# Kernel optimization log

Hardware: AMD Instinct MI355X
Metric: run time of the kernel (lower is better)

The kernel has to match this reference:

```python
import jax, jax.numpy as jnp
import numpy as np

HEADS = 8
DIM_HEAD = 64
NB_FEATURES = 256
CHUNK = 128          # chunk size used by performer's causal_linear_attention_noncuda
EPS_KERNEL = 1e-4    # eps in softmax_kernel feature map
EPS_DENOM = 1e-6     # eps added to k_cumsum in the denominator


def softmax_kernel(data, proj, is_query):
    # FAVOR+ positive softmax random features (performer_pytorch.softmax_kernel)
    # data: [B,H,N,D], proj: [M,D]
    d = data.shape[-1]
    normalizer = d ** -0.25
    ratio = proj.shape[0] ** -0.5
    data_dash = jnp.einsum('bhnd,md->bhnm', data * normalizer, proj)
    # ||x||^2 / (2*sqrt(d))
    diag = jnp.sum(data * data, axis=-1, keepdims=True) * 0.5 * (normalizer ** 2)
    if is_query:
        m = jax.lax.stop_gradient(jnp.max(data_dash, axis=-1, keepdims=True))
    else:
        m = jax.lax.stop_gradient(jnp.max(data_dash, axis=(-1, -2), keepdims=True))
    return ratio * (jnp.exp(data_dash - diag - m) + EPS_KERNEL)


def causal_linear_attention(qp, kp, v, chunk=CHUNK):
    # Chunked causal linear attention (O(N) in seq len):
    # out_i = q'_i . S_i / (q'_i . z_i), S_i = sum_{j<=i} k'_j v_j^T, z_i = cumsum k'_j
    B, H, N, M = qp.shape
    E = v.shape[-1]
    C = N // chunk

    def to_chunks(x):
        return x.reshape(B, H, C, chunk, x.shape[-1]).transpose(2, 0, 1, 3, 4)

    qc, kc, vc = to_chunks(qp), to_chunks(kp), to_chunks(v)
    k0 = jnp.zeros((B, H, M), qp.dtype)
    s0 = jnp.zeros((B, H, M, E), qp.dtype)

    def step(carry, inp):
        k_last, s_last = carry
        q, k, vv = inp  # [B,H,c,M], [B,H,c,M], [B,H,c,E]
        k_cum = k_last[:, :, None, :] + jnp.cumsum(k, axis=2)           # [B,H,c,M]
        d_inv = 1.0 / jnp.einsum('bhnm,bhnm->bhn', q, k_cum + EPS_DENOM)
        ctx = jnp.einsum('bhnm,bhne->bhnme', k, vv)                      # [B,H,c,M,E]
        s_cum = s_last[:, :, None] + jnp.cumsum(ctx, axis=2)             # [B,H,c,M,E]
        out = jnp.einsum('bhnme,bhnm,bhn->bhne', s_cum, q, d_inv)        # [B,H,c,E]
        return (k_cum[:, :, -1, :], s_cum[:, :, -1]), out

    _, outs = jax.lax.scan(step, (k0, s0), (qc, kc, vc))  # [C,B,H,c,E]
    return outs.transpose(1, 2, 0, 3, 4).reshape(B, H, N, E)


def setup_inputs() -> dict:
    key = jax.random.key(0)
    k1, k2, k3, k4 = jax.random.split(key, 4)
    B, N, D = 4, 2048, 512
    return {
        'query': jax.random.normal(k1, (B, N, D), jnp.float32),
        'key': jax.random.normal(k2, (B, N, D), jnp.float32),
        'value': jax.random.normal(k3, (B, N, D), jnp.float32),
        'projection': jax.random.normal(k4, (NB_FEATURES, DIM_HEAD), jnp.float32),
    }


def reference(query, key, value, projection):
    B, N, D = query.shape

    def split(x):  # [B,N,D] -> [B,H,N,Dh]
        return x.reshape(B, N, HEADS, DIM_HEAD).transpose(0, 2, 1, 3)

    q, k, v = split(query), split(key), split(value)
    qp = softmax_kernel(q, projection, is_query=True)
    kp = softmax_kernel(k, projection, is_query=False)
    out = causal_linear_attention(qp, kp, v)
    return out.transpose(0, 2, 1, 3).reshape(B, N, D)
```

## Files before the change

kernel.cpp:

```cpp
#include <hip/hip_runtime.h>
#include <math.h>

#define BB 4
#define NN 2048
#define DD 512
#define HH 8
#define DH 64
#define MM 256
#define BH 32
#define CHK 128
#define NCH 16
#define ROWS (BH*NN)

constexpr float NRM   = 0.35355339059327373f;
constexpr float RATIO = 0.0625f;
constexpr float EPSK  = 1e-4f;
constexpr float EPSD  = 1e-6f;

#define OFFB_QP   ((size_t)0)
#define OFFB_SP   ((size_t)33554432)
#define OFFB_KP   (OFFB_SP + (size_t)16777216)
#define OFFB_VT   (OFFB_KP + (size_t)33554432)
#define OFFB_Z    (OFFB_VT + (size_t)8388608)
#define OFFB_KMP  (OFFB_Z  + (size_t)524288)
#define OFFB_KMAX (OFFB_KMP + (size_t)4096)

typedef __attribute__((ext_vector_type(8))) short short8;
typedef __attribute__((ext_vector_type(4))) float f32x4;

__device__ __forceinline__ float b2f(ushort u) {
  union { float f; unsigned int i; } x; x.i = ((unsigned int)u) << 16; return x.f;
}
__device__ __forceinline__ ushort f2b(float f) {
  unsigned int u = __float_as_uint(f);
  unsigned int r = (u + 0x7FFFu + ((u >> 16) & 1u)) >> 16;
  return (ushort)r;
}

#define MFMA(a,b,c) __builtin_amdgcn_mfma_f32_16x16x32_bf16(a, b, c, 0, 0, 0)

template<int MODE>
__global__ __launch_bounds__(256) void featm_kernel(const float* __restrict__ inp,
                                                    const float* __restrict__ proj,
                                                    char* __restrict__ ws) {
  __shared__ __align__(16) char lds[55296];
  __shared__ float diag_s[64];
  __shared__ __align__(16) float wmax[64][4];
  __shared__ float kred[4];

  ushort* xh = (ushort*)lds;
  ushort* xl = xh + 64*72;
  ushort* ps = xl + 64*72;
  ushort* qt = ps;

  const int t  = threadIdx.x;
  const int w  = t >> 6;
  const int l  = t & 63;
  const int lq = l >> 4;
  const int ln = l & 15;

  const int rowbase = blockIdx.x * 64;
  const int bh = rowbase >> 11;
  const int b  = bh >> 3, h = bh & 7;
  const int n0 = rowbase & (NN - 1);

  {
    const int r  = t >> 2;
    const int c0 = (t & 3) * 16;
    const float* src = inp + ((size_t)(b*NN + n0 + r))*DD + h*DH + c0;
    float vv[16];
    #pragma unroll
    for (int j = 0; j < 4; ++j) {
      float4 v = *(const float4*)(src + j*4);
      vv[4*j+0] = v.x*NRM; vv[4*j+1] = v.y*NRM;
      vv[4*j+2] = v.z*NRM; vv[4*j+3] = v.w*NRM;
    }
    float s = 0.f;
    ushort hi[16], lo[16];
    #pragma unroll
    for (int j = 0; j < 16; ++j) {
      s += vv[j]*vv[j];
      hi[j] = f2b(vv[j]);
      lo[j] = f2b(vv[j] - b2f(hi[j]));
    }
    *(short8*)(xh + r*72 + c0)     = *(short8*)&hi[0];
    *(short8*)(xh + r*72 + c0 + 8) = *(short8*)&hi[8];
    *(short8*)(xl + r*72 + c0)     = *(short8*)&lo[0];
    *(short8*)(xl + r*72 + c0 + 8) = *(short8*)&lo[8];
    s += __shfl_xor(s, 1); s += __shfl_xor(s, 2);
    if ((t & 3) == 0) diag_s[r] = 0.5f * s;
  }
  #pragma unroll
  for (int ld = 0; ld < 4; ++ld) {
    int flat = t + 256*ld;
    int r = flat >> 2, c0 = (flat & 3) * 16;
    const float* src = proj + (size_t)r*DH + c0;
    ushort hv[16];
    #pragma unroll
    for (int j = 0; j < 4; ++j) {
      float4 v = *(const float4*)(src + j*4);
      hv[4*j+0] = f2b(v.x); hv[4*j+1] = f2b(v.y);
      hv[4*j+2] = f2b(v.z); hv[4*j+3] = f2b(v.w);
    }
    *(short8*)(ps + r*72 + c0)     = *(short8*)&hv[0];
    *(short8*)(ps + r*72 + c0 + 8) = *(short8*)&hv[8];
  }
  __syncthreads();

  f32x4 acc[4][4];
  #pragma unroll
  for (int mt = 0; mt < 4; ++mt)
    #pragma unroll
    for (int nt = 0; nt < 4; ++nt) acc[mt][nt] = (f32x4){0.f,0.f,0.f,0.f};

  #pragma unroll
  for (int kk = 0; kk < 2; ++kk) {
    short8 ah[4], al[4];
    #pragma unroll
    for (int mt = 0; mt < 4; ++mt) {
      ah[mt] = *(const short8*)(xh + (mt*16 + ln)*72 + kk*32 + lq*8);
      al[mt] = *(const short8*)(xl + (mt*16 + ln)*72 + kk*32 + lq*8);
    }
    #pragma unroll
    for (int nt = 0; nt < 4; ++nt) {
      short8 bf = *(const short8*)(ps + (w*64 + nt*16 + ln)*72 + kk*32 + lq*8);
      #pragma unroll
      for (int mt = 0; mt < 4; ++mt) {
        acc[mt][nt] = MFMA(al[mt], bf, acc[mt][nt]);
        acc[mt][nt] = MFMA(ah[mt], bf, acc[mt][nt]);
      }
    }
  }

  if (MODE == 1) {
    float mx = -1e30f;
    #pragma unroll
    for (int mt = 0; mt < 4; ++mt)
      #pragma unroll
      for (int nt = 0; nt < 4; ++nt)
        #pragma unroll
        for (int reg = 0; reg < 4; ++reg) mx = fmaxf(mx, acc[mt][nt][reg]);
    #pragma unroll
    for (int m = 1; m < 64; m <<= 1) mx = fmaxf(mx, __shfl_xor(mx, m));
    if (l == 0) kred[w] = mx;
    __syncthreads();
    if (t == 0)
      ((float*)(ws + OFFB_KMP))[blockIdx.x] =
        fmaxf(fmaxf(kred[0], kred[1]), fmaxf(kred[2], kred[3]));
    return;
  }

  if (MODE == 0) {
    #pragma unroll
    for (int mt = 0; mt < 4; ++mt)
      #pragma unroll
      for (int reg = 0; reg < 4; ++reg) {
        float m = acc[mt][0][reg];
        #pragma unroll
        for (int nt = 1; nt < 4; ++nt) m = fmaxf(m, acc[mt][nt][reg]);
        m = fmaxf(m, __shfl_xor(m, 1));
        m = fmaxf(m, __shfl_xor(m, 2));
        m = fmaxf(m, __shfl_xor(m, 4));
        m = fmaxf(m, __shfl_xor(m, 8));
        if (ln == 0) wmax[mt*16 + lq*4 + reg][w] = m;
      }
  }
  __syncthreads();

  float km = 0.f;
  if (MODE == 2) km = ((const float*)(ws + OFFB_KMAX))[bh];

  #pragma unroll
  for (int mt = 0; mt < 4; ++mt)
    #pragma unroll
    for (int reg = 0; reg < 4; ++reg) {
      const int row = mt*16 + lq*4 + reg;
      float rm;
      if (MODE == 0) {
        float4 wm4 = *(const float4*)&wmax[row][0];
        rm = fmaxf(fmaxf(wm4.x, wm4.y), fmaxf(wm4.z, wm4.w));
      } else {
        rm = km;
      }
      const float dg = diag_s[row];
      #pragma unroll
      for (int nt = 0; nt < 4; ++nt)
        qt[row*264 + w*64 + nt*16 + ln] =
          f2b(RATIO*(expf(acc[mt][nt][reg] - dg - rm) + EPSK));
    }
  __syncthreads();

  ushort* dstbase = (ushort*)(ws + (MODE == 0 ? OFFB_QP : OFFB_KP)) + (size_t)rowbase*MM;
  #pragma unroll
  for (int ld = 0; ld < 8; ++ld) {
    int flat = t + 256*ld;
    int row = flat >> 5, g = flat & 31;
    *(short8*)(dstbase + (size_t)row*MM + g*8) = *(const short8*)(qt + row*264 + g*8);
  }
}

__global__ void kmax_kernel(char* __restrict__ ws) {
  const int t = threadIdx.x;
  if (t < BH) {
    const float* kmp = (const float*)(ws + OFFB_KMP);
    float m = -1e30f;
    for (int i = 0; i < 32; ++i) m = fmaxf(m, kmp[t*32 + i]);
    ((float*)(ws + OFFB_KMAX))[t] = m;
  }
}

__global__ __launch_bounds__(256) void vt_kernel(const float* __restrict__ value,
                                                 char* __restrict__ ws) {
  __shared__ __align__(16) float vsh[128][68];
  const int t = threadIdx.x;
  const int bh = blockIdx.x >> 4, nc = blockIdx.x & 15;
  const int b = bh >> 3, h = bh & 7;
  const int n0 = nc * CHK;
  #pragma unroll
  for (int l = 0; l < 8; ++l) {
    int flat = t + 256*l;
    int r = flat >> 4, g = flat & 15;
    *(float4*)&vsh[r][g*4] = *(const float4*)(value + ((size_t)(b*NN + n0 + r))*DD + h*DH + g*4);
  }
  __syncthreads();
  const int e = t & 63, qd = t >> 6;
  ushort* vt = (ushort*)(ws + OFFB_VT) + ((size_t)bh*DH + e)*NN + n0 + qd*32;
  #pragma unroll
  for (int p = 0; p < 16; ++p) {
    unsigned int lo = f2b(vsh[qd*32 + 2*p][e]);
    unsigned int hi = f2b(vsh[qd*32 + 2*p + 1][e]);
    ((unsigned int*)vt)[p] = lo | (hi << 16);
  }
}

__global__ __launch_bounds__(256) void sprefix_kernel(char* __restrict__ ws) {
  __shared__ __align__(16) unsigned int kpTu[64*68];
  __shared__ __align__(16) ushort Vts[64*136];
  __shared__ float zred[4][64];

  const int t  = threadIdx.x;
  const int w  = t >> 6;
  const int l  = t & 63;
  const int lq = l >> 4;
  const int ln = l & 15;
  const int bh = blockIdx.x >> 2;
  const int ms = blockIdx.x & 3;

  const ushort* kpb = (const ushort*)(ws + OFFB_KP) + (size_t)bh*NN*MM + ms*64;
  const ushort* vtb = (const ushort*)(ws + OFFB_VT) + (size_t)bh*DH*NN;
  ushort* spb = (ushort*)(ws + OFFB_SP) + (size_t)bh*NCH*DH*MM + ms*64;
  float*  zb  = (float*)(ws + OFFB_Z) + (size_t)bh*NCH*MM + ms*64;

  f32x4 acc[4];
  #pragma unroll
  for (int nt = 0; nt < 4; ++nt) acc[nt] = (f32x4){0.f,0.f,0.f,0.f};
  float zrun = 0.f;

  for (int tc = 0; tc < NCH; ++tc) {
    __syncthreads();

    if (t < 64) {
      if (tc > 0) zrun += zred[0][t] + zred[1][t] + zred[2][t] + zred[3][t];
      zb[(size_t)tc*MM + t] = zrun;
    }
    {
      ushort* sp = spb + (size_t)tc*DH*MM;
      #pragma unroll
      for (int nt = 0; nt < 4; ++nt)
        #pragma unroll
        for (int reg = 0; reg < 4; ++reg)
          sp[(size_t)(w*16 + lq*4 + reg)*MM + nt*16 + ln] = f2b(acc[nt][reg]);
    }

    const ushort* kslice = kpb + (size_t)tc*CHK*MM;
    #pragma unroll
    for (int it = 0; it < 2; ++it) {
      int slot = t + 256*it;
      int jp = slot >> 3, mo = slot & 7;
      short8 a = *(const short8*)(kslice + (size_t)(2*jp)*MM + mo*8);
      short8 c = *(const short8*)(kslice + (size_t)(2*jp+1)*MM + mo*8);
      #pragma unroll
      for (int i = 0; i < 8; ++i) {
        unsigned int u = (unsigned int)(unsigned short)a[i]
                       | ((unsigned int)(unsigned short)c[i] << 16);
        kpTu[(mo*8 + i)*68 + jp] = u;
      }
    }
    #pragma unroll
    for (int it = 0; it < 4; ++it) {
      int slot = t + 256*it;
      int e = slot >> 4, g = slot & 15;
      *(short8*)(Vts + e*136 + g*8) = *(const short8*)(vtb + (size_t)e*NN + tc*CHK + g*8);
    }
    __syncthreads();

    {
      int m = t & 63, q = t >> 6;
      float s = 0.f;
      #pragma unroll
      for (int u = 0; u < 16; ++u) {
        unsigned int p = kpTu[m*68 + q*16 + u];
        s += b2f((ushort)(p & 0xFFFF)) + b2f((ushort)(p >> 16));
      }
      zred[q][m] = s;
    }

    #pragma unroll
    for (int kk = 0; kk < 4; ++kk) {
      short8 af = *(const short8*)(Vts + (w*16 + ln)*136 + kk*32 + lq*8);
      #pragma unroll
      for (int nt = 0; nt < 4; ++nt) {
        short8 bf = *(const short8*)((const ushort*)kpTu + ((size_t)(nt*16 + ln)*68 + kk*16 + lq*4)*2);
        acc[nt] = MFMA(af, bf, acc[nt]);
      }
    }
  }
}

__global__ __launch_bounds__(256) void fused_kernel(float* __restrict__ out,
                                                    char* __restrict__ ws) {
  __shared__ __align__(16) char lds[52224];
  __shared__ float den_i[128];
  __shared__ float dinv_s[128];

  const int t  = threadIdx.x;
  const int w  = t >> 6;
  const int l  = t & 63;
  const int lq = l >> 4;
  const int ln = l & 15;
  const int blk = blockIdx.x;
  const int bh = blk >> 4, tc = blk & 15;
  const int b = bh >> 3, h = bh & 7;
  const size_t rowbase = (size_t)bh*NN + tc*CHK;

  const ushort* qpg = (const ushort*)(ws + OFFB_QP) + rowbase*MM;
  const ushort* kpg = (const ushort*)(ws + OFFB_KP) + rowbase*MM;

  ushort* qs = (ushort*)lds;
  ushort* ks = qs + 128*72;

  f32x4 acc[2][8];
  #pragma unroll
  for (int mt = 0; mt < 2; ++mt)
    #pragma unroll
    for (int nt = 0; nt < 8; ++nt) acc[mt][nt] = (f32x4){0.f,0.f,0.f,0.f};

  const int ntmax = 2*w + 2;

  for (int mc = 0; mc < 4; ++mc) {
    __syncthreads();
    #pragma unroll
    for (int ld2 = 0; ld2 < 4; ++ld2) {
      int flat = t + 256*ld2; int r = flat >> 3, g = flat & 7;
      *(short8*)(qs + r*72 + g*8) = *(const short8*)(qpg + (size_t)r*MM + mc*64 + g*8);
      *(short8*)(ks + r*72 + g*8) = *(const short8*)(kpg + (size_t)r*MM + mc*64 + g*8);
    }
    __syncthreads();
    #pragma unroll
    for (int kk = 0; kk < 2; ++kk) {
      short8 af0 = *(const short8*)(qs + (w*32 +      ln)*72 + kk*32 + lq*8);
      short8 af1 = *(const short8*)(qs + (w*32 + 16 + ln)*72 + kk*32 + lq*8);
      #pragma unroll
      for (int nt = 0; nt < 8; ++nt) {
        if (nt < ntmax) {
          short8 bf = *(const short8*)(ks + (nt*16 + ln)*72 + kk*32 + lq*8);
          acc[0][nt] = MFMA(af0, bf, acc[0][nt]);
          acc[1][nt] = MFMA(af1, bf, acc[1][nt]);
        }
      }
    }
  }

  __syncthreads();

  ushort* P   = (ushort*)lds;
  ushort* Vts = (ushort*)(lds + 34816);

  float rs[2][4] = {{0,0,0,0},{0,0,0,0}};
  #pragma unroll
  for (int mt = 0; mt < 2; ++mt)
    #pragma unroll
    for (int nt = 0; nt < 8; ++nt)
      #pragma unroll
      for (int reg = 0; reg < 4; ++reg) {
        int i = w*32 + mt*16 + lq*4 + reg;
        int j = nt*16 + ln;
        float v = (j <= i) ? acc[mt][nt][reg] : 0.f;
        rs[mt][reg] += v;
        P[i*136 + j] = f2b(v);
      }
  #pragma unroll
  for (int mt = 0; mt < 2; ++mt)
    #pragma unroll
    for (int reg = 0; reg < 4; ++reg) {
      float s = rs[mt][reg];
      s += __shfl_xor(s, 1); s += __shfl_xor(s, 2);
      s += __shfl_xor(s, 4); s += __shfl_xor(s, 8);
      if (ln == 0) den_i[w*32 + mt*16 + lq*4 + reg] = s;
    }

  const ushort* vtg = (const ushort*)(ws + OFFB_VT) + (size_t)bh*DH*NN + tc*CHK;
  #pragma unroll
  for (int ld2 = 0; ld2 < 4; ++ld2) {
    int flat = t + 256*ld2; int e = flat >> 4, g = flat & 15;
    *(short8*)(Vts + e*136 + g*8) = *(const short8*)(vtg + (size_t)e*NN + g*8);
  }
  __syncthreads();

  {
    const float* zp = (const float*)(ws + OFFB_Z) + (size_t)blk*MM;
    const int r = t >> 1, hf = t & 1;
    const ushort* qrow = qpg + (size_t)r*MM + hf*128;
    float s = 0.f;
    #pragma unroll
    for (int g = 0; g < 16; ++g) {
      short8 qv = *(const short8*)(qrow + g*8);
      const float* zz = zp + hf*128 + g*8;
      #pragma unroll
      for (int x = 0; x < 8; ++x)
        s += b2f((ushort)qv[x]) * (zz[x] + EPSD);
    }
    s += __shfl_xor(s, 1);
    if (hf == 0) dinv_s[r] = 1.0f / (s + den_i[r]);
  }

  f32x4 oacc[2][4];
  #pragma unroll
  for (int mt = 0; mt < 2; ++mt)
    #pragma unroll
    for (int nt = 0; nt < 4; ++nt) oacc[mt][nt] = (f32x4){0.f,0.f,0.f,0.f};

  #pragma unroll
  for (int kk = 0; kk < 4; ++kk) {
    short8 af0 = *(const short8*)(P + (w*32 +      ln)*136 + kk*32 + lq*8);
    short8 af1 = *(const short8*)(P + (w*32 + 16 + ln)*136 + kk*32 + lq*8);
    #pragma unroll
    for (int nt = 0; nt < 4; ++nt) {
      short8 bf = *(const short8*)(Vts + (nt*16 + ln)*136 + kk*32 + lq*8);
      oacc[0][nt] = MFMA(af0, bf, oacc[0][nt]);
      oacc[1][nt] = MFMA(af1, bf, oacc[1][nt]);
    }
  }
  __syncthreads();

  ushort* qs2 = (ushort*)lds;
  ushort* ss  = qs2 + 128*72;
  const ushort* spg = (const ushort*)(ws + OFFB_SP) + (size_t)blk*DH*MM;
  for (int mc = 0; mc < 4; ++mc) {
    if (mc) __syncthreads();
    #pragma unroll
    for (int ld2 = 0; ld2 < 4; ++ld2) {
      int flat = t + 256*ld2; int r = flat >> 3, g = flat & 7;
      *(short8*)(qs2 + r*72 + g*8) = *(const short8*)(qpg + (size_t)r*MM + mc*64 + g*8);
    }
    #pragma unroll
    for (int ld2 = 0; ld2 < 2; ++ld2) {
      int flat = t + 256*ld2; int e = flat >> 3, g = flat & 7;
      *(short8*)(ss + e*72 + g*8) = *(const short8*)(spg + (size_t)e*MM + mc*64 + g*8);
    }
    __syncthreads();
    #pragma unroll
    for (int kk = 0; kk < 2; ++kk) {
      short8 af0 = *(const short8*)(qs2 + (w*32 +      ln)*72 + kk*32 + lq*8);
      short8 af1 = *(const short8*)(qs2 + (w*32 + 16 + ln)*72 + kk*32 + lq*8);
      #pragma unroll
      for (int nt = 0; nt < 4; ++nt) {
        short8 bf = *(const short8*)(ss + (nt*16 + ln)*72 + kk*32 + lq*8);
        oacc[0][nt] = MFMA(af0, bf, oacc[0][nt]);
        oacc[1][nt] = MFMA(af1, bf, oacc[1][nt]);
      }
    }
  }

  #pragma unroll
  for (int mt = 0; mt < 2; ++mt)
    #pragma unroll
    for (int reg = 0; reg < 4; ++reg) {
      const int i = w*32 + mt*16 + lq*4 + reg;
      const float di = dinv_s[i];
      float* dst = out + ((size_t)(b*NN) + tc*CHK + i)*DD + h*DH;
      #pragma unroll
      for (int nt = 0; nt < 4; ++nt)
        dst[nt*16 + ln] = oacc[mt][nt][reg] * di;
    }
}

extern "C" void kernel_launch(void* const* d_in, const int* in_sizes, int n_in,
                              void* d_out, int out_size, void* d_ws, size_t ws_size,
                              hipStream_t stream) {
  (void)in_sizes; (void)n_in; (void)out_size; (void)ws_size;
  const float* q    = (const float*)d_in[0];
  const float* k    = (const float*)d_in[1];
  const float* v    = (const float*)d_in[2];
  const float* proj = (const float*)d_in[3];
  float* out = (float*)d_out;
  char*  ws  = (char*)d_ws;

  featm_kernel<0><<<1024, 256, 0, stream>>>(q, proj, ws);
  featm_kernel<1><<<1024, 256, 0, stream>>>(k, proj, ws);
  kmax_kernel<<<1, 256, 0, stream>>>(ws);
  featm_kernel<2><<<1024, 256, 0, stream>>>(k, proj, ws);
  vt_kernel<<<512, 256, 0, stream>>>(v, ws);
  sprefix_kernel<<<128, 256, 0, stream>>>(ws);
  fused_kernel<<<512, 256, 0, stream>>>(out, ws);
}
```

Before: 203.8 us.

## Merge feature/value kernels, fold kmax reduction, split sprefix finer, balance causal tiles

Merges the query-feature, key-max and value-transpose launches into one mega kernel and folds the per-head key max reduction into the second key-feature pass, which removes two launches and a one-block serial kernel. Doubles the sprefix grid by giving each block 32 features instead of 64, so more CUs work on the sequential chunk scan. In the fused kernel each wave now takes row tiles w and 7-w, which evens out the causal triangle work across waves. The costs are extra LDS pointer arithmetic, a larger shared allocation for the merged kernel, and duplicated V loads across the finer sprefix blocks.

Measured after the change: 194.9 us. 1.05x faster.

```diff
diff --git a/kernel.cpp b/kernel.cpp
--- a/kernel.cpp
+++ b/kernel.cpp
@@ -23,7 +23,6 @@
 #define OFFB_VT   (OFFB_KP + (size_t)33554432)
 #define OFFB_Z    (OFFB_VT + (size_t)8388608)
 #define OFFB_KMP  (OFFB_Z  + (size_t)524288)
-#define OFFB_KMAX (OFFB_KMP + (size_t)4096)
 
 typedef __attribute__((ext_vector_type(8))) short short8;
 typedef __attribute__((ext_vector_type(4))) float f32x4;
@@ -40,18 +39,17 @@
 #define MFMA(a,b,c) __builtin_amdgcn_mfma_f32_16x16x32_bf16(a, b, c, 0, 0, 0)
 
 template<int MODE>
-__global__ __launch_bounds__(256) void featm_kernel(const float* __restrict__ inp,
-                                                    const float* __restrict__ proj,
-                                                    char* __restrict__ ws) {
-  __shared__ __align__(16) char lds[55296];
-  __shared__ float diag_s[64];
-  __shared__ __align__(16) float wmax[64][4];
-  __shared__ float kred[4];
-
+__device__ __forceinline__ void featm_body(const float* __restrict__ inp,
+                                           const float* __restrict__ proj,
+                                           char* __restrict__ ws,
+                                           char* lds, int blk) {
   ushort* xh = (ushort*)lds;
   ushort* xl = xh + 64*72;
   ushort* ps = xl + 64*72;
   ushort* qt = ps;
+  float* diag_s = (float*)(lds + 55296);
+  float (*wmax)[4] = (float(*)[4])(lds + 55552);
+  float* kred = (float*)(lds + 56576);
 
   const int t  = threadIdx.x;
   const int w  = t >> 6;
@@ -59,7 +57,7 @@
   const int lq = l >> 4;
   const int ln = l & 15;
 
-  const int rowbase = blockIdx.x * 64;
+  const int rowbase = blk * 64;
   const int bh = rowbase >> 11;
   const int b  = bh >> 3, h = bh & 7;
   const int n0 = rowbase & (NN - 1);
@@ -145,7 +143,7 @@
     if (l == 0) kred[w] = mx;
     __syncthreads();
     if (t == 0)
-      ((float*)(ws + OFFB_KMP))[blockIdx.x] =
+      ((float*)(ws + OFFB_KMP))[blk] =
         fmaxf(fmaxf(kred[0], kred[1]), fmaxf(kred[2], kred[3]));
     return;
   }
@@ -165,10 +163,18 @@
         if (ln == 0) wmax[mt*16 + lq*4 + reg][w] = m;
       }
   }
+  if (MODE == 2) {
+    if (t < 32) {
+      float m = ((const float*)(ws + OFFB_KMP))[bh*32 + t];
+      #pragma unroll
+      for (int d = 1; d < 32; d <<= 1) m = fmaxf(m, __shfl_xor(m, d));
+      if (t == 0) kred[0] = m;
+    }
+  }
   __syncthreads();
 
   float km = 0.f;
-  if (MODE == 2) km = ((const float*)(ws + OFFB_KMAX))[bh];
+  if (MODE == 2) km = kred[0];
 
   #pragma unroll
   for (int mt = 0; mt < 4; ++mt)
@@ -199,21 +205,12 @@
   }
 }
 
-__global__ void kmax_kernel(char* __restrict__ ws) {
+__device__ __forceinline__ void vt_body(const float* __restrict__ value,
+                                        char* __restrict__ ws,
+                                        char* lds, int blk) {
+  float (*vsh)[68] = (float(*)[68])lds;
   const int t = threadIdx.x;
-  if (t < BH) {
-    const float* kmp = (const float*)(ws + OFFB_KMP);
-    float m = -1e30f;
-    for (int i = 0; i < 32; ++i) m = fmaxf(m, kmp[t*32 + i]);
-    ((float*)(ws + OFFB_KMAX))[t] = m;
-  }
-}
-
-__global__ __launch_bounds__(256) void vt_kernel(const float* __restrict__ value,
-                                                 char* __restrict__ ws) {
-  __shared__ __align__(16) float vsh[128][68];
-  const int t = threadIdx.x;
-  const int bh = blockIdx.x >> 4, nc = blockIdx.x & 15;
+  const int bh = blk >> 4, nc = blk & 15;
   const int b = bh >> 3, h = bh & 7;
   const int n0 = nc * CHK;
   #pragma unroll
@@ -233,50 +230,72 @@
   }
 }
 
+__global__ __launch_bounds__(256) void mega_kernel(const float* __restrict__ q,
+                                                   const float* __restrict__ k,
+                                                   const float* __restrict__ v,
+                                                   const float* __restrict__ proj,
+                                                   char* __restrict__ ws) {
+  __shared__ __align__(16) char lds[56832];
+  const int blk = blockIdx.x;
+  if (blk < 1024)       featm_body<0>(q, proj, ws, lds, blk);
+  else if (blk < 2048)  featm_body<1>(k, proj, ws, lds, blk - 1024);
+  else                  vt_body(v, ws, lds, blk - 2048);
+}
+
+__global__ __launch_bounds__(256) void featm2_kernel(const float* __restrict__ k,
+                                                     const float* __restrict__ proj,
+                                                     char* __restrict__ ws) {
+  __shared__ __align__(16) char lds[56832];
+  featm_body<2>(k, proj, ws, lds, blockIdx.x);
+}
+
 __global__ __launch_bounds__(256) void sprefix_kernel(char* __restrict__ ws) {
-  __shared__ __align__(16) unsigned int kpTu[64*68];
+  __shared__ __align__(16) unsigned int kpTu[32*68];
   __shared__ __align__(16) ushort Vts[64*136];
-  __shared__ float zred[4][64];
+  __shared__ float zred[8][32];
 
   const int t  = threadIdx.x;
   const int w  = t >> 6;
   const int l  = t & 63;
   const int lq = l >> 4;
   const int ln = l & 15;
-  const int bh = blockIdx.x >> 2;
-  const int ms = blockIdx.x & 3;
-
-  const ushort* kpb = (const ushort*)(ws + OFFB_KP) + (size_t)bh*NN*MM + ms*64;
+  const int bh = blockIdx.x >> 3;
+  const int ms = blockIdx.x & 7;
+
+  const ushort* kpb = (const ushort*)(ws + OFFB_KP) + (size_t)bh*NN*MM + ms*32;
   const ushort* vtb = (const ushort*)(ws + OFFB_VT) + (size_t)bh*DH*NN;
-  ushort* spb = (ushort*)(ws + OFFB_SP) + (size_t)bh*NCH*DH*MM + ms*64;
-  float*  zb  = (float*)(ws + OFFB_Z) + (size_t)bh*NCH*MM + ms*64;
-
-  f32x4 acc[4];
-  #pragma unroll
-  for (int nt = 0; nt < 4; ++nt) acc[nt] = (f32x4){0.f,0.f,0.f,0.f};
+  ushort* spb = (ushort*)(ws + OFFB_SP) + (size_t)bh*NCH*DH*MM + ms*32;
+  float*  zb  = (float*)(ws + OFFB_Z) + (size_t)bh*NCH*MM + ms*32;
+
+  f32x4 acc[2];
+  acc[0] = (f32x4){0.f,0.f,0.f,0.f};
+  acc[1] = (f32x4){0.f,0.f,0.f,0.f};
   float zrun = 0.f;
 
   for (int tc = 0; tc < NCH; ++tc) {
     __syncthreads();
 
-    if (t < 64) {
-      if (tc > 0) zrun += zred[0][t] + zred[1][t] + zred[2][t] + zred[3][t];
+    if (t < 32) {
+      if (tc > 0) {
+        float s = 0.f;
+        #pragma unroll
+        for (int q = 0; q < 8; ++q) s += zred[q][t];
+        zrun += s;
+      }
       zb[(size_t)tc*MM + t] = zrun;
     }
     {
       ushort* sp = spb + (size_t)tc*DH*MM;
       #pragma unroll
-      for (int nt = 0; nt < 4; ++nt)
+      for (int nt = 0; nt < 2; ++nt)
         #pragma unroll
         for (int reg = 0; reg < 4; ++reg)
           sp[(size_t)(w*16 + lq*4 + reg)*MM + nt*16 + ln] = f2b(acc[nt][reg]);
     }
 
     const ushort* kslice = kpb + (size_t)tc*CHK*MM;
-    #pragma unroll
-    for (int it = 0; it < 2; ++it) {
-      int slot = t + 256*it;
-      int jp = slot >> 3, mo = slot & 7;
+    {
+      int jp = t >> 2, mo = t & 3;
       short8 a = *(const short8*)(kslice + (size_t)(2*jp)*MM + mo*8);
       short8 c = *(const short8*)(kslice + (size_t)(2*jp+1)*MM + mo*8);
       #pragma unroll
@@ -295,11 +314,11 @@
     __syncthreads();
 
     {
-      int m = t & 63, q = t >> 6;
+      int m = t & 31, q = t >> 5;
       float s = 0.f;
       #pragma unroll
-      for (int u = 0; u < 16; ++u) {
-        unsigned int p = kpTu[m*68 + q*16 + u];
+      for (int u = 0; u < 8; ++u) {
+        unsigned int p = kpTu[m*68 + q*8 + u];
         s += b2f((ushort)(p & 0xFFFF)) + b2f((ushort)(p >> 16));
       }
       zred[q][m] = s;
@@ -309,8 +328,8 @@
     for (int kk = 0; kk < 4; ++kk) {
       short8 af = *(const short8*)(Vts + (w*16 + ln)*136 + kk*32 + lq*8);
       #pragma unroll
-      for (int nt = 0; nt < 4; ++nt) {
-        short8 bf = *(const short8*)((const ushort*)kpTu + ((size_t)(nt*16 + ln)*68 + kk*16 + lq*4)*2);
+      for (int nt = 0; nt < 2; ++nt) {
+        short8 bf = *(const short8*)((const ushort*)kpTu + (size_t)(nt*16 + ln)*136 + kk*32 + lq*8);
         acc[nt] = MFMA(af, bf, acc[nt]);
       }
     }
@@ -328,6 +347,8 @@
   const int l  = t & 63;
   const int lq = l >> 4;
   const int ln = l & 15;
+  const int rt0 = w;
+  const int rt1 = 7 - w;
   const int blk = blockIdx.x;
   const int bh = blk >> 4, tc = blk & 15;
   const int b = bh >> 3, h = bh & 7;
@@ -345,8 +366,6 @@
     #pragma unroll
     for (int nt = 0; nt < 8; ++nt) acc[mt][nt] = (f32x4){0.f,0.f,0.f,0.f};
 
-  const int ntmax = 2*w + 2;
-
   for (int mc = 0; mc < 4; ++mc) {
     __syncthreads();
     #pragma unroll
@@ -358,13 +377,13 @@
     __syncthreads();
     #pragma unroll
     for (int kk = 0; kk < 2; ++kk) {
-      short8 af0 = *(const short8*)(qs + (w*32 +      ln)*72 + kk*32 + lq*8);
-      short8 af1 = *(const short8*)(qs + (w*32 + 16 + ln)*72 + kk*32 + lq*8);
+      short8 af0 = *(const short8*)(qs + (rt0*16 + ln)*72 + kk*32 + lq*8);
+      short8 af1 = *(const short8*)(qs + (rt1*16 + ln)*72 + kk*32 + lq*8);
       #pragma unroll
       for (int nt = 0; nt < 8; ++nt) {
-        if (nt < ntmax) {
+        if (nt <= rt1) {
           short8 bf = *(const short8*)(ks + (nt*16 + ln)*72 + kk*32 + lq*8);
-          acc[0][nt] = MFMA(af0, bf, acc[0][nt]);
+          if (nt <= rt0) acc[0][nt] = MFMA(af0, bf, acc[0][nt]);
           acc[1][nt] = MFMA(af1, bf, acc[1][nt]);
         }
       }
@@ -378,26 +397,30 @@
 
   float rs[2][4] = {{0,0,0,0},{0,0,0,0}};
   #pragma unroll
-  for (int mt = 0; mt < 2; ++mt)
+  for (int mt = 0; mt < 2; ++mt) {
+    const int ibase = (mt ? rt1 : rt0) * 16;
     #pragma unroll
     for (int nt = 0; nt < 8; ++nt)
       #pragma unroll
       for (int reg = 0; reg < 4; ++reg) {
-        int i = w*32 + mt*16 + lq*4 + reg;
+        int i = ibase + lq*4 + reg;
         int j = nt*16 + ln;
         float v = (j <= i) ? acc[mt][nt][reg] : 0.f;
         rs[mt][reg] += v;
         P[i*136 + j] = f2b(v);
       }
-  #pragma unroll
-  for (int mt = 0; mt < 2; ++mt)
+  }
+  #pragma unroll
+  for (int mt = 0; mt < 2; ++mt) {
+    const int ibase = (mt ? rt1 : rt0) * 16;
     #pragma unroll
     for (int reg = 0; reg < 4; ++reg) {
       float s = rs[mt][reg];
       s += __shfl_xor(s, 1); s += __shfl_xor(s, 2);
       s += __shfl_xor(s, 4); s += __shfl_xor(s, 8);
-      if (ln == 0) den_i[w*32 + mt*16 + lq*4 + reg] = s;
-    }
+      if (ln == 0) den_i[ibase + lq*4 + reg] = s;
+    }
+  }
 
   const ushort* vtg = (const ushort*)(ws + OFFB_VT) + (size_t)bh*DH*NN + tc*CHK;
   #pragma unroll
@@ -432,8 +455,8 @@
 
   #pragma unroll
   for (int kk = 0; kk < 4; ++kk) {
-    short8 af0 = *(const short8*)(P + (w*32 +      ln)*136 + kk*32 + lq*8);
-    short8 af1 = *(const short8*)(P + (w*32 + 16 + ln)*136 + kk*32 + lq*8);
+    short8 af0 = *(const short8*)(P + (rt0*16 + ln)*136 + kk*32 + lq*8);
+    short8 af1 = *(const short8*)(P + (rt1*16 + ln)*136 + kk*32 + lq*8);
     #pragma unroll
     for (int nt = 0; nt < 4; ++nt) {
       short8 bf = *(const short8*)(Vts + (nt*16 + ln)*136 + kk*32 + lq*8);
@@ -461,8 +484,8 @@
     __syncthreads();
     #pragma unroll
     for (int kk = 0; kk < 2; ++kk) {
-      short8 af0 = *(const short8*)(qs2 + (w*32 +      ln)*72 + kk*32 + lq*8);
-      short8 af1 = *(const short8*)(qs2 + (w*32 + 16 + ln)*72 + kk*32 + lq*8);
+      short8 af0 = *(const short8*)(qs2 + (rt0*16 + ln)*72 + kk*32 + lq*8);
+      short8 af1 = *(const short8*)(qs2 + (rt1*16 + ln)*72 + kk*32 + lq*8);
       #pragma unroll
       for (int nt = 0; nt < 4; ++nt) {
         short8 bf = *(const short8*)(ss + (nt*16 + ln)*72 + kk*32 + lq*8);
@@ -473,16 +496,18 @@
   }
 
   #pragma unroll
-  for (int mt = 0; mt < 2; ++mt)
+  for (int mt = 0; mt < 2; ++mt) {
+    const int ibase = (mt ? rt1 : rt0) * 16;
     #pragma unroll
     for (int reg = 0; reg < 4; ++reg) {
-      const int i = w*32 + mt*16 + lq*4 + reg;
+      const int i = ibase + lq*4 + reg;
       const float di = dinv_s[i];
       float* dst = out + ((size_t)(b*NN) + tc*CHK + i)*DD + h*DH;
       #pragma unroll
       for (int nt = 0; nt < 4; ++nt)
         dst[nt*16 + ln] = oacc[mt][nt][reg] * di;
     }
+  }
 }
 
 extern "C" void kernel_launch(void* const* d_in, const int* in_sizes, int n_in,
@@ -496,11 +521,8 @@
   float* out = (float*)d_out;
   char*  ws  = (char*)d_ws;
 
-  featm_kernel<0><<<1024, 256, 0, stream>>>(q, proj, ws);
-  featm_kernel<1><<<1024, 256, 0, stream>>>(k, proj, ws);
-  kmax_kernel<<<1, 256, 0, stream>>>(ws);
-  featm_kernel<2><<<1024, 256, 0, stream>>>(k, proj, ws);
-  vt_kernel<<<512, 256, 0, stream>>>(v, ws);
-  sprefix_kernel<<<128, 256, 0, stream>>>(ws);
+  mega_kernel<<<2560, 256, 0, stream>>>(q, k, v, proj, ws);
+  featm2_kernel<<<1024, 256, 0, stream>>>(k, proj, ws);
+  sprefix_kernel<<<256, 256, 0, stream>>>(ws);
   fused_kernel<<<512, 256, 0, stream>>>(out, ws);
 }
```
